# Optimization experiments

Measured on AMD Instinct MI355X. Metric: run time of the kernel, lower is better.

The kernel has to match this reference:

```python
import jax, jax.numpy as jnp
import numpy as np

D_MODEL = 768
KERNELS = [7, 5, 3]
FILTERS = [40, 30, 20]
FC_IN = sum(FILTERS)  # 90


def setup_inputs() -> dict:
    key = jax.random.key(0)
    ks = jax.random.split(key, 16)
    B, S, D = 8, 2048, D_MODEL
    inp = {
        'x1': jax.random.normal(ks[0], (B, S, D), jnp.float32),
        'x2': jax.random.normal(ks[1], (B, S, D), jnp.float32),
    }
    # conv weights: OIH layout [out_ch, in_ch, k]
    for i, (k, f) in enumerate(zip(KERNELS, FILTERS)):
        scale = 1.0 / np.sqrt(D * k)
        inp[f'w{k}'] = jax.random.uniform(ks[2 + 2 * i], (f, D, k), jnp.float32, -scale, scale)
        inp[f'b{k}'] = jax.random.uniform(ks[3 + 2 * i], (f,), jnp.float32, -scale, scale)
    inp['U'] = jax.random.normal(ks[8], (D, D), jnp.float32) * (1.0 / np.sqrt(D))
    inp['bias_v'] = jax.random.normal(ks[9], (D,), jnp.float32) * 0.02
    inp['fc_w'] = jax.random.normal(ks[10], (D, FC_IN), jnp.float32) * (1.0 / np.sqrt(FC_IN))
    inp['fc_b'] = jnp.zeros((D,), jnp.float32)
    inp['fcx_w'] = jax.random.normal(ks[11], (D, 2 * D), jnp.float32) * (1.0 / np.sqrt(2 * D))
    inp['fcx_b'] = jnp.zeros((D,), jnp.float32)
    return inp


def _conv1d_same(x_ncs, w_oik, b_o, k):
    # x: [B, C, S], w: [O, C, k] -> [B, O, S], 'same' padding = k//2
    y = jax.lax.conv_general_dilated(
        x_ncs, w_oik, window_strides=(1,), padding=[(k // 2, k // 2)],
        dimension_numbers=('NCH', 'OIH', 'NCH'))
    return y + b_o[None, :, None]


def reference(x1, x2, w7, b7, w5, b5, w3, b3, U, bias_v, fc_w, fc_b, fcx_w, fcx_b):
    # CNN branch over x2 (dropout layers are identity in eval mode)
    xc = jnp.transpose(x2, (0, 2, 1))  # [B, D, S]
    feats = jnp.concatenate([
        jnp.transpose(_conv1d_same(xc, w7, b7, 7), (0, 2, 1)),
        jnp.transpose(_conv1d_same(xc, w5, b5, 5), (0, 2, 1)),
        jnp.transpose(_conv1d_same(xc, w3, b3, 3), (0, 2, 1)),
    ], axis=-1)                                    # [B, S, 90]
    x = jnp.tanh(jax.nn.relu(feats) @ fc_w.T + fc_b)  # [B, S, D]
    # biaffine attention: x1 @ U @ x2^T + x2 @ bias (broadcast over rows)
    attn = jnp.einsum('bsd,de,bte->bst', x1, U, x2) + (x2 @ bias_v)[:, None, :]
    attn = jax.nn.softmax(attn, axis=-1)           # [B, S, S]
    out = jnp.tanh(attn @ x2)                      # [B, S, D]
    x = x + out
    return jnp.concatenate([x1, x], axis=-1) @ fcx_w.T + fcx_b  # [B, S, D]
```

## Files before the change

### kernel.cpp

```cpp
#include <hip/hip_runtime.h>
#include <cmath>

#define D_MODEL 768
#define SEQ 2048
#define BATCH 8
#define FC_PAD 96
#define FC_PAD2 128
#define KCOMB (7 * D_MODEL)
#define KCHUNK 2688
#define NT_SC (D_MODEL / 64)

typedef unsigned short ushort_t;
typedef _Float16 half_t;
typedef __attribute__((ext_vector_type(8))) _Float16 f16x8;
typedef __attribute__((ext_vector_type(8))) unsigned short u16x8;
typedef __attribute__((ext_vector_type(4))) unsigned short u16x4;
typedef __attribute__((ext_vector_type(4))) float f32x4;

struct Ptr8 { const ushort_t* p[8]; };

__device__ __forceinline__ ushort_t f2h(float x) {
    half_t h = (half_t)x;
    return __builtin_bit_cast(ushort_t, h);
}
__device__ __forceinline__ float h2f(ushort_t u) {
    return (float)__builtin_bit_cast(half_t, u);
}
__device__ __forceinline__ float fast_tanh(float x) {
    float a = fabsf(x);
    float t = __expf(-2.f * a);
    float r = (1.f - t) / (1.f + t);
    return copysignf(r, x);
}
__device__ __forceinline__ void gload16(const ushort_t* g, ushort_t* lbase) {
    __builtin_amdgcn_global_load_lds((const __attribute__((address_space(1))) void*)g,
                                     (__attribute__((address_space(3))) void*)lbase,
                                     16, 0, 0);
}

__global__ void convert_f16_kernel(const float* __restrict__ src, ushort_t* __restrict__ dst, size_t n4) {
    size_t i = (size_t)blockIdx.x * 256 + threadIdx.x;
    if (i >= n4) return;
    f32x4 x = *(const f32x4*)(src + i * 4);
    u16x4 h;
    #pragma unroll
    for (int j = 0; j < 4; ++j) h[j] = f2h(x[j]);
    *(u16x4*)(dst + i * 4) = h;
}

__global__ void convert_fc_kernel(const float* __restrict__ src, ushort_t* __restrict__ dst) {
    int i = blockIdx.x * 256 + threadIdx.x;
    if (i >= D_MODEL * FC_PAD2) return;
    int o = i / FC_PAD2, j = i - o * FC_PAD2;
    dst[i] = (j < 90) ? f2h(src[o * 90 + j]) : 0;
}

__global__ void convert_ut_kernel(const float* __restrict__ U, ushort_t* __restrict__ dst) {
    int i = blockIdx.x * 256 + threadIdx.x;
    if (i >= D_MODEL * D_MODEL) return;
    int n = i / D_MODEL, k = i - n * D_MODEL;
    dst[i] = f2h(U[(size_t)k * D_MODEL + n]);
}

__global__ void build_wcomb_kernel(const float* __restrict__ w7, const float* __restrict__ b7,
                                   const float* __restrict__ w5, const float* __restrict__ b5,
                                   const float* __restrict__ w3, const float* __restrict__ b3,
                                   ushort_t* __restrict__ Wt, float* __restrict__ bcat) {
    int idx = blockIdx.x * 256 + threadIdx.x;
    const int total = FC_PAD2 * KCOMB;
    if (idx < total) {
        int o = idx / KCOMB, k = idx - o * KCOMB;
        int t = k / D_MODEL, d = k - t * D_MODEL;
        float v = 0.f;
        if (o < 40) {
            v = w7[(size_t)o * (D_MODEL * 7) + d * 7 + t];
        } else if (o < 70) {
            int t5 = t - 1;
            if (t5 >= 0 && t5 < 5) v = w5[(size_t)(o - 40) * (D_MODEL * 5) + d * 5 + t5];
        } else if (o < 90) {
            int t3 = t - 2;
            if (t3 >= 0 && t3 < 3) v = w3[(size_t)(o - 70) * (D_MODEL * 3) + d * 3 + t3];
        }
        Wt[idx] = f2h(v);
    }
    if (idx < FC_PAD2) {
        float bv = 0.f;
        if (idx < 40) bv = b7[idx];
        else if (idx < 70) bv = b5[idx - 40];
        else if (idx < 90) bv = b3[idx - 70];
        bcat[idx] = bv;
    }
}

__global__ void conv_reduce_kernel(const float* __restrict__ P, const float* __restrict__ bcat,
                                   ushort_t* __restrict__ feats) {
    const size_t MT = (size_t)BATCH * SEQ;
    size_t i = (size_t)blockIdx.x * 256 + threadIdx.x;
    if (i >= MT * FC_PAD2) return;
    int col = (int)(i & (FC_PAD2 - 1));
    size_t row = i >> 7;
    float v = 0.f;
    if (col < FC_PAD) {
        size_t idx = row * FC_PAD + col;
        const size_t st = MT * FC_PAD;
        v = P[idx] + P[idx + st] + bcat[col];
        v = fmaxf(v, 0.f);
    }
    feats[i] = f2h(v);
}

__global__ void transpose_f16_kernel(const ushort_t* __restrict__ in, ushort_t* __restrict__ out) {
    __shared__ ushort_t tile[32][40];
    int b = blockIdx.z;
    int s0 = blockIdx.x * 32, d0 = blockIdx.y * 32;
    int tx = threadIdx.x & 31, ty = threadIdx.x >> 5;
    const ushort_t* inb = in + (size_t)b * SEQ * D_MODEL;
    ushort_t* outb = out + (size_t)b * D_MODEL * SEQ;
    #pragma unroll
    for (int i = 0; i < 4; ++i)
        tile[ty + i * 8][tx] = inb[(size_t)(s0 + ty + i * 8) * D_MODEL + d0 + tx];
    __syncthreads();
    #pragma unroll
    for (int i = 0; i < 4; ++i)
        outb[(size_t)(d0 + ty + i * 8) * SEQ + s0 + tx] = tile[tx][ty + i * 8];
}

__global__ __launch_bounds__(512, 2)
void scores_kernel(const ushort_t* __restrict__ Abase, const ushort_t* __restrict__ Bbase,
                   Ptr8 ap, float* __restrict__ smw, float* __restrict__ slw) {
    __shared__ __align__(16) ushort_t As_[2][2][256][32];
    __shared__ __align__(16) ushort_t Bs_[2][2][256][32];
    __shared__ float pmW[4][256];
    __shared__ float msS[256];
    __shared__ float plW[4][256];

    const int lin = blockIdx.x;
    const int z = lin & 7;
    const int t6 = lin >> 3;
    const int bx = t6 & 7, by = t6 >> 3;
    const ushort_t* A = Abase + (size_t)z * SEQ * D_MODEL;
    const ushort_t* B = Bbase + (size_t)z * SEQ * D_MODEL;
    const int m0 = bx * 256, n0 = by * 256;

    const int tid = threadIdx.x;
    const int lane = tid & 63;
    const int wave = tid >> 6;
    const int wm2 = wave >> 2;
    const int wn4 = wave & 3;
    const int r16 = lane & 15, kq = lane >> 4;
    const int srow = tid >> 2;
    const int sslot = tid & 3;

    auto swz3 = [](int row) { return (row & 3) ^ ((row >> 2) & 1); };

    auto STAGE = [&](int buf, int kh, int kbase) {
        #pragma unroll
        for (int i = 0; i < 2; ++i) {
            int row = i * 128 + srow;
            int gk = kbase + kh * 32 + ((sslot ^ swz3(row)) << 3);
            gload16(A + (size_t)(m0 + row) * D_MODEL + gk, &As_[buf][kh][i * 128 + wave * 16][0]);
        }
        #pragma unroll
        for (int i = 0; i < 2; ++i) {
            int row = i * 128 + srow;
            int gk = kbase + kh * 32 + ((sslot ^ swz3(row)) << 3);
            gload16(B + (size_t)(n0 + row) * D_MODEL + gk, &Bs_[buf][kh][i * 128 + wave * 16][0]);
        }
    };

    f32x4 acc[8][4];
    #pragma unroll
    for (int i = 0; i < 8; ++i)
        #pragma unroll
        for (int j = 0; j < 4; ++j) acc[i][j] = (f32x4){0.f, 0.f, 0.f, 0.f};

    STAGE(0, 0, 0);
    STAGE(0, 1, 0);
    asm volatile("s_waitcnt vmcnt(0)" ::: "memory");
    __builtin_amdgcn_sched_barrier(0);
    __builtin_amdgcn_s_barrier();
    __builtin_amdgcn_sched_barrier(0);

    for (int t = 0; t < NT_SC; ++t) {
        const int buf = t & 1;
        const int kbn = (t + 1) * 64;
        #pragma unroll
        for (int kk = 0; kk < 2; ++kk) {
            f16x8 af[8], bf[4];
            #pragma unroll
            for (int mi = 0; mi < 8; ++mi) {
                int row = wm2 * 128 + mi * 16 + r16;
                af[mi] = *(const f16x8*)&As_[buf][kk][row][(kq ^ swz3(row)) << 3];
            }
            #pragma unroll
            for (int ni = 0; ni < 4; ++ni) {
                int row = wn4 * 64 + ni * 16 + r16;
                bf[ni] = *(const f16x8*)&Bs_[buf][kk][row][(kq ^ swz3(row)) << 3];
            }
            if (t + 1 < NT_SC) STAGE(buf ^ 1, kk, kbn);
            asm volatile("s_waitcnt vmcnt(4)" ::: "memory");
            asm volatile("s_waitcnt lgkmcnt(0)" ::: "memory");
            __builtin_amdgcn_sched_barrier(0);
            __builtin_amdgcn_s_setprio(1);
            #pragma unroll
            for (int mi = 0; mi < 8; ++mi)
                #pragma unroll
                for (int ni = 0; ni < 4; ++ni)
                    acc[mi][ni] = __builtin_amdgcn_mfma_f32_16x16x32_f16(af[mi], bf[ni], acc[mi][ni], 0, 0, 0);
            __builtin_amdgcn_s_setprio(0);
            __builtin_amdgcn_sched_barrier(0);
            __builtin_amdgcn_s_barrier();
            __builtin_amdgcn_sched_barrier(0);
        }
    }

    float red[8][4];
    #pragma unroll
    for (int mi = 0; mi < 8; ++mi)
        #pragma unroll
        for (int r = 0; r < 4; ++r) {
            float mx = fmaxf(fmaxf(acc[mi][0][r], acc[mi][1][r]), fmaxf(acc[mi][2][r], acc[mi][3][r]));
            mx = fmaxf(mx, __shfl_xor(mx, 1));
            mx = fmaxf(mx, __shfl_xor(mx, 2));
            mx = fmaxf(mx, __shfl_xor(mx, 4));
            mx = fmaxf(mx, __shfl_xor(mx, 8));
            red[mi][r] = mx;
        }
    if (r16 == 0) {
        #pragma unroll
        for (int mi = 0; mi < 8; ++mi)
            #pragma unroll
            for (int r = 0; r < 4; ++r)
                pmW[wn4][wm2 * 128 + mi * 16 + kq * 4 + r] = red[mi][r];
    }
    __syncthreads();
    if (tid < 256)
        msS[tid] = fmaxf(fmaxf(pmW[0][tid], pmW[1][tid]), fmaxf(pmW[2][tid], pmW[3][tid]));
    __syncthreads();
    #pragma unroll
    for (int mi = 0; mi < 8; ++mi)
        #pragma unroll
        for (int r = 0; r < 4; ++r) {
            float m = msS[wm2 * 128 + mi * 16 + kq * 4 + r];
            float s = 0.f;
            #pragma unroll
            for (int ni = 0; ni < 4; ++ni) {
                float e = __expf(acc[mi][ni][r] - m);
                acc[mi][ni][r] = e;
                s += e;
            }
            s += __shfl_xor(s, 1);
            s += __shfl_xor(s, 2);
            s += __shfl_xor(s, 4);
            s += __shfl_xor(s, 8);
            red[mi][r] = s;
        }
    if (r16 == 0) {
        #pragma unroll
        for (int mi = 0; mi < 8; ++mi)
            #pragma unroll
            for (int r = 0; r < 4; ++r)
                plW[wn4][wm2 * 128 + mi * 16 + kq * 4 + r] = red[mi][r];
    }
    __syncthreads();
    if (tid < 256) {
        float l = plW[0][tid] + plW[1][tid] + plW[2][tid] + plW[3][tid];
        size_t si = ((size_t)z * 8 + by) * SEQ + (m0 + tid);
        smw[si] = msS[tid];
        slw[si] = l;
    }
    ushort_t* Co = (ushort_t*)ap.p[z];
    #pragma unroll
    for (int mi = 0; mi < 8; ++mi)
        #pragma unroll
        for (int ni = 0; ni < 4; ++ni)
            #pragma unroll
            for (int r = 0; r < 4; ++r) {
                int gm = m0 + wm2 * 128 + mi * 16 + kq * 4 + r;
                int gn = n0 + wn4 * 64 + ni * 16 + r16;
                Co[(size_t)gm * SEQ + gn] = f2h(acc[mi][ni][r]);
            }
}

template<int TM, int TN, int AMODE, int ACT, int HASBIAS, int HASADD,
         int OUTMODE, int KSPLIT, int APTR, int MAP, int ZM, int GX, int GY,
         int ASCALE>
__global__ __launch_bounds__(256, 4)
void mfma_gemm(const ushort_t* __restrict__ A, const ushort_t* __restrict__ A2,
               const ushort_t* __restrict__ B, const float* __restrict__ bias,
               const ushort_t* __restrict__ addsrc,
               float* __restrict__ Cf, ushort_t* __restrict__ Ch,
               Ptr8 ap, const float* __restrict__ smw, const float* __restrict__ slw,
               int M, int N, int K, int lda, int ldb, int ldc,
               size_t sA, size_t sB, size_t sBias, size_t sC) {
    constexpr int WM = TM / 2, WN = TN / 2, FM = WM / 16, FN = WN / 16;
    __shared__ __align__(16) ushort_t As_[TM * 64];
    __shared__ __align__(16) ushort_t Bs_[TN * 64];
    __shared__ ushort_t alS[ASCALE ? 8 : 1][ASCALE ? 128 : 1];

    int bx, by, z;
    if (MAP == 1) {
        int lin = blockIdx.x;
        z = lin % ZM;
        int t = lin / ZM;
        bx = t % GX;
        by = t / GX;
    } else if (MAP == 2) {
        int lin = blockIdx.x;
        int xcd = lin & 7;
        int t = lin >> 3;
        by = t % GY;
        bx = xcd * (GX / 8) + t / GY;
        z = 0;
    } else if (MAP == 3) {
        int lin = blockIdx.x;
        z = lin % ZM;
        int t = lin / ZM;
        by = t % GY;
        bx = t / GY;
    } else {
        bx = blockIdx.x; by = blockIdx.y; z = blockIdx.z;
    }

    const int kb = KSPLIT ? z * K : 0;
    const ushort_t* Ab = APTR ? ap.p[z] : (A + (KSPLIT ? 0 : (size_t)z * sA));
    const ushort_t* Bb = B + (KSPLIT ? 0 : (size_t)z * sB);
    if (HASBIAS) bias += (size_t)z * sBias;
    if (HASADD) addsrc += (size_t)z * sC;
    if (OUTMODE == 0) Cf += (size_t)z * sC;
    else Ch += (size_t)z * sC;

    const int m0 = bx * TM;
    const int n0 = by * TN;
    const int tid = threadIdx.x;
    const int lane = tid & 63;
    const int wave = tid >> 6;
    const int wm = (wave >> 1) * WM, wn = (wave & 1) * WN;
    const int r16 = lane & 15, kq = lane >> 4;
    const int srow = tid >> 3;
    const int slot = tid & 7;

    if (ASCALE) {
        if (tid < 128) {
            int row = tid;
            int gm = m0 + row;
            float mt[8], al[8];
            float mg = -3.0e38f;
            #pragma unroll
            for (int t = 0; t < 8; ++t) {
                mt[t] = smw[((size_t)z * 8 + t) * SEQ + gm];
                mg = fmaxf(mg, mt[t]);
            }
            float lg = 0.f;
            #pragma unroll
            for (int t = 0; t < 8; ++t) {
                float e = __expf(mt[t] - mg);
                lg += slw[((size_t)z * 8 + t) * SEQ + gm] * e;
                al[t] = e;
            }
            float inv = 1.f / lg;
            #pragma unroll
            for (int t = 0; t < 8; ++t) alS[t][row] = f2h(al[t] * inv);
        }
        __syncthreads();
    }

    f32x4 acc[FM][FN];
    #pragma unroll
    for (int i = 0; i < FM; ++i)
        #pragma unroll
        for (int j = 0; j < FN; ++j) acc[i][j] = (f32x4){0.f, 0.f, 0.f, 0.f};

    const u16x8 zv = {0, 0, 0, 0, 0, 0, 0, 0};

    for (int k0 = 0; k0 < K; k0 += 64) {
        #pragma unroll
        for (int i = 0; i < TM / 32; ++i) {
            int row = i * 32 + srow;
            int gm = m0 + row;
            int xs = slot ^ (row & 7);
            if (AMODE == 1) {
                int gkk = kb + k0 + xs * 8;
                int t = gkk / D_MODEL, d = gkk - t * D_MODEL;
                int s = (gm & (SEQ - 1)) + t - 3;
                int bb = gm >> 11;
                u16x8 v = (s >= 0 && s < SEQ) ? *(const u16x8*)(Ab + ((size_t)(bb * SEQ + s)) * lda + d) : zv;
                *(u16x8*)&As_[(size_t)row * 64 + slot * 8] = v;
            } else {
                const ushort_t* src;
                if (AMODE == 2) {
                    int gk = k0 + xs * 8;
                    src = (gk < D_MODEL) ? Ab + (size_t)gm * D_MODEL + gk
                                         : A2 + (size_t)gm * D_MODEL + (gk - D_MODEL);
                } else {
                    int gk = kb + k0 + xs * 8;
                    src = Ab + (size_t)gm * lda + gk;
                }
                gload16(src, &As_[(size_t)(i * 32 + wave * 8) * 64]);
            }
        }
        #pragma unroll
        for (int i = 0; i < TN / 32; ++i) {
            int row = i * 32 + srow;
            int gn = n0 + row;
            int xs = slot ^ (row & 7);
            int gk = kb + k0 + xs * 8;
            gload16(Bb + (size_t)gn * ldb + gk, &Bs_[(size_t)(i * 32 + wave * 8) * 64]);
        }
        __syncthreads();

        f16x8 ah[FM][2], bh[FN][2];
        #pragma unroll
        for (int mi = 0; mi < FM; ++mi) {
            int row = wm + mi * 16 + r16;
            #pragma unroll
            for (int kk = 0; kk < 2; ++kk)
                ah[mi][kk] = *(const f16x8*)&As_[(size_t)row * 64 + (((kk * 4 + kq) ^ (row & 7)) * 8)];
        }
        if (ASCALE) {
            const int kt = k0 >> 8;
            #pragma unroll
            for (int mi = 0; mi < FM; ++mi) {
                half_t s = __builtin_bit_cast(half_t, alS[kt][wm + mi * 16 + r16]);
                ah[mi][0] = ah[mi][0] * s;
                ah[mi][1] = ah[mi][1] * s;
            }
        }
        #pragma unroll
        for (int ni = 0; ni < FN; ++ni) {
            int row = wn + ni * 16 + r16;
            #pragma unroll
            for (int kk = 0; kk < 2; ++kk)
                bh[ni][kk] = *(const f16x8*)&Bs_[(size_t)row * 64 + (((kk * 4 + kq) ^ (row & 7)) * 8)];
        }
        #pragma unroll
        for (int kk = 0; kk < 2; ++kk)
            #pragma unroll
            for (int mi = 0; mi < FM; ++mi)
                #pragma unroll
                for (int ni = 0; ni < FN; ++ni)
                    acc[mi][ni] = __builtin_amdgcn_mfma_f32_16x16x32_f16(ah[mi][kk], bh[ni][kk], acc[mi][ni], 0, 0, 0);
        __syncthreads();
    }

    #pragma unroll
    for (int mi = 0; mi < FM; ++mi)
        #pragma unroll
        for (int ni = 0; ni < FN; ++ni)
            #pragma unroll
            for (int r = 0; r < 4; ++r) {
                int gm = m0 + wm + mi * 16 + kq * 4 + r;
                int gn = n0 + wn + ni * 16 + r16;
                if (gn >= N) continue;
                float v = acc[mi][ni][r];
                if (HASBIAS) v += bias[gn];
                if (ACT == 1) v = fmaxf(v, 0.f);
                else if (ACT == 2) v = fast_tanh(v);
                if (HASADD) v += h2f(addsrc[(size_t)gm * ldc + gn]);
                size_t idx = (size_t)gm * ldc + gn;
                if (OUTMODE == 0) Cf[idx] = v;
                else Ch[idx] = f2h(v);
            }
}

extern "C" void kernel_launch(void* const* d_in, const int* in_sizes, int n_in,
                              void* d_out, int out_size, void* d_ws, size_t ws_size,
                              hipStream_t stream) {
    const float* x1     = (const float*)d_in[0];
    const float* x2     = (const float*)d_in[1];
    const float* w7     = (const float*)d_in[2];
    const float* b7     = (const float*)d_in[3];
    const float* w5     = (const float*)d_in[4];
    const float* b5     = (const float*)d_in[5];
    const float* w3     = (const float*)d_in[6];
    const float* b3     = (const float*)d_in[7];
    const float* U      = (const float*)d_in[8];
    const float* bias_v = (const float*)d_in[9];
    const float* fc_w   = (const float*)d_in[10];
    const float* fc_b   = (const float*)d_in[11];
    const float* fcx_w  = (const float*)d_in[12];
    const float* fcx_b  = (const float*)d_in[13];
    float* out = (float*)d_out;

    const size_t MT = (size_t)BATCH * SEQ;
    const size_t NE = MT * D_MODEL;
    const size_t NEb = (size_t)SEQ * D_MODEL;
    const size_t SEGSZ = (size_t)SEQ * SEQ;

    char* p = (char*)d_ws;
    auto alloc = [&](size_t bytes) -> char* {
        char* r = p;
        p += (bytes + 255) & ~(size_t)255;
        return r;
    };
    ushort_t* x1_h   = (ushort_t*)alloc(NE * 2);
    ushort_t* x2_h   = (ushort_t*)alloc(NE * 2);
    ushort_t* x2t    = (ushort_t*)alloc(NE * 2);
    ushort_t* y1     = (ushort_t*)alloc(NE * 2);
    ushort_t* xcnn   = (ushort_t*)alloc(NE * 2);
    float*    convp  = (float*)   alloc(MT * FC_PAD * 4 * 4);
    ushort_t* feats  = (ushort_t*)alloc(MT * FC_PAD2 * 2);
    ushort_t* Wt     = (ushort_t*)alloc((size_t)FC_PAD2 * KCOMB * 2);
    ushort_t* fc_wt  = (ushort_t*)alloc((size_t)D_MODEL * FC_PAD2 * 2);
    ushort_t* fcx_wt = (ushort_t*)alloc((size_t)D_MODEL * 2 * D_MODEL * 2);
    ushort_t* Ut     = (ushort_t*)alloc((size_t)D_MODEL * D_MODEL * 2);
    float*    bcat   = (float*)alloc(FC_PAD2 * 4);
    float*    smS    = (float*)alloc((size_t)BATCH * 8 * SEQ * 4);
    float*    slS    = (float*)alloc((size_t)BATCH * 8 * SEQ * 4);

    ushort_t* dob = (ushort_t*)d_out;
    Ptr8 ap;
    ap.p[0] = (ushort_t*)convp;
    ap.p[1] = (ushort_t*)convp + SEGSZ;
    ap.p[2] = (ushort_t*)convp + 2 * SEGSZ;
    ap.p[3] = dob;
    ap.p[4] = dob + SEGSZ;
    ap.p[5] = dob + 2 * SEGSZ;
    ap.p[6] = dob + 3 * SEGSZ;
    ap.p[7] = dob + 4 * SEGSZ;
    Ptr8 apz = {};

    const int T = 256;
    auto blk = [](size_t n) { return dim3((unsigned)((n + 255) / 256)); };

    build_wcomb_kernel<<<blk((size_t)FC_PAD2 * KCOMB), T, 0, stream>>>(w7, b7, w5, b5, w3, b3, Wt, bcat);
    convert_fc_kernel<<<blk((size_t)D_MODEL * FC_PAD2), T, 0, stream>>>(fc_w, fc_wt);
    convert_f16_kernel<<<blk((size_t)D_MODEL * 2 * D_MODEL / 4), T, 0, stream>>>(fcx_w, fcx_wt, (size_t)D_MODEL * 2 * D_MODEL / 4);
    convert_ut_kernel<<<blk((size_t)D_MODEL * D_MODEL), T, 0, stream>>>(U, Ut);
    convert_f16_kernel<<<blk(NE / 4), T, 0, stream>>>(x1, x1_h, NE / 4);
    convert_f16_kernel<<<blk(NE / 4), T, 0, stream>>>(x2, x2_h, NE / 4);
    transpose_f16_kernel<<<dim3(SEQ / 32, D_MODEL / 32, BATCH), T, 0, stream>>>(x2_h, x2t);

    mfma_gemm<64, 128, 1, 0, 0, 0, 0, 1, 0, 0, 1, 1, 1, 0><<<dim3(MT / 64, 1, 2), T, 0, stream>>>(
        x2_h, nullptr, Wt, nullptr, nullptr,
        convp, nullptr, apz, nullptr, nullptr,
        (int)MT, FC_PAD, KCHUNK, D_MODEL, KCOMB, FC_PAD,
        0, 0, 0, MT * FC_PAD);
    conv_reduce_kernel<<<blk(MT * FC_PAD2), T, 0, stream>>>(convp, bcat, feats);

    mfma_gemm<128, 128, 0, 2, 1, 0, 1, 0, 0, 2, 1, 128, 6, 0><<<dim3(768, 1, 1), T, 0, stream>>>(
        feats, nullptr, fc_wt, fc_b, nullptr,
        nullptr, xcnn, apz, nullptr, nullptr,
        (int)MT, D_MODEL, FC_PAD2, FC_PAD2, FC_PAD2, D_MODEL, 0, 0, 0, 0);

    mfma_gemm<128, 128, 0, 0, 1, 0, 1, 0, 0, 2, 1, 128, 6, 0><<<dim3(768, 1, 1), T, 0, stream>>>(
        x1_h, nullptr, Ut, bias_v, nullptr,
        nullptr, y1, apz, nullptr, nullptr,
        (int)MT, D_MODEL, D_MODEL, D_MODEL, D_MODEL, D_MODEL, 0, 0, 0, 0);

    scores_kernel<<<dim3(512, 1, 1), dim3(512), 0, stream>>>(y1, x2_h, ap, smS, slS);

    mfma_gemm<128, 128, 0, 2, 0, 1, 1, 0, 1, 3, 8, 16, 6, 1><<<dim3(768, 1, 1), T, 0, stream>>>(
        nullptr, nullptr, x2t, nullptr,
        xcnn,
        nullptr, xcnn, ap, smS, slS,
        SEQ, D_MODEL, SEQ, SEQ, SEQ, D_MODEL,
        0, NEb, 0, NEb);

    mfma_gemm<128, 128, 2, 0, 1, 0, 0, 0, 0, 2, 1, 128, 6, 0><<<dim3(768, 1, 1), T, 0, stream>>>(
        x1_h, xcnn, fcx_wt, fcx_b, nullptr,
        out, nullptr, apz, nullptr, nullptr,
        (int)MT, D_MODEL, 2 * D_MODEL, D_MODEL, 2 * D_MODEL, D_MODEL, 0, 0, 0, 0);
}
```

Baseline: 346.7 us.

## Retile scores kernel to 256x128 with triple-buffered 64-wide K pipeline

The scores GEMM tile shrinks from 256x256 to 256x128, which doubles the grid to 1024 blocks. The K loop now stages full 64-wide slices into a three-deep LDS ring with XOR swizzle, so loads run two tiles ahead. Partial softmax statistics now come in 16 column chunks instead of 8, and the consumer GEMM's per-chunk scale logic is updated to match. In exchange, each wave holds fewer accumulators and does less operand reuse, there is more partial-stat traffic, and launch bounds drop to one block per CU.

```diff
diff --git a/kernel.cpp b/kernel.cpp
--- a/kernel.cpp
+++ b/kernel.cpp
@@ -8,7 +8,7 @@
 #define FC_PAD2 128
 #define KCOMB (7 * D_MODEL)
 #define KCHUNK 2688
-#define NT_SC (D_MODEL / 64)
+#define NKT 12
 
 typedef unsigned short ushort_t;
 typedef _Float16 half_t;
@@ -125,14 +125,14 @@
         outb[(size_t)(d0 + ty + i * 8) * SEQ + s0 + tx] = tile[tx][ty + i * 8];
 }
 
-__global__ __launch_bounds__(512, 2)
+__global__ __launch_bounds__(512, 1)
 void scores_kernel(const ushort_t* __restrict__ Abase, const ushort_t* __restrict__ Bbase,
                    Ptr8 ap, float* __restrict__ smw, float* __restrict__ slw) {
-    __shared__ __align__(16) ushort_t As_[2][2][256][32];
-    __shared__ __align__(16) ushort_t Bs_[2][2][256][32];
-    __shared__ float pmW[4][256];
+    __shared__ __align__(16) ushort_t As_[3][256][64];
+    __shared__ __align__(16) ushort_t Bs_[3][128][64];
+    __shared__ float pmW[2][256];
     __shared__ float msS[256];
-    __shared__ float plW[4][256];
+    __shared__ float plW[2][256];
 
     const int lin = blockIdx.x;
     const int z = lin & 7;
@@ -140,83 +140,89 @@
     const int bx = t6 & 7, by = t6 >> 3;
     const ushort_t* A = Abase + (size_t)z * SEQ * D_MODEL;
     const ushort_t* B = Bbase + (size_t)z * SEQ * D_MODEL;
-    const int m0 = bx * 256, n0 = by * 256;
+    const int m0 = bx * 256, n0 = by * 128;
 
     const int tid = threadIdx.x;
     const int lane = tid & 63;
     const int wave = tid >> 6;
-    const int wm2 = wave >> 2;
-    const int wn4 = wave & 3;
+    const int wm4 = wave >> 1;
+    const int wn2 = wave & 1;
     const int r16 = lane & 15, kq = lane >> 4;
-    const int srow = tid >> 2;
-    const int sslot = tid & 3;
-
-    auto swz3 = [](int row) { return (row & 3) ^ ((row >> 2) & 1); };
-
-    auto STAGE = [&](int buf, int kh, int kbase) {
+    const int srow = tid >> 3;
+    const int slot = tid & 7;
+
+    auto STAGE = [&](int buf, int kt) {
+        #pragma unroll
+        for (int i = 0; i < 4; ++i) {
+            int row = i * 64 + srow;
+            int xs = slot ^ (row & 7);
+            gload16(A + (size_t)(m0 + row) * D_MODEL + kt * 64 + xs * 8,
+                    &As_[buf][i * 64 + wave * 8][0]);
+        }
         #pragma unroll
         for (int i = 0; i < 2; ++i) {
-            int row = i * 128 + srow;
-            int gk = kbase + kh * 32 + ((sslot ^ swz3(row)) << 3);
-            gload16(A + (size_t)(m0 + row) * D_MODEL + gk, &As_[buf][kh][i * 128 + wave * 16][0]);
-        }
-        #pragma unroll
-        for (int i = 0; i < 2; ++i) {
-            int row = i * 128 + srow;
-            int gk = kbase + kh * 32 + ((sslot ^ swz3(row)) << 3);
-            gload16(B + (size_t)(n0 + row) * D_MODEL + gk, &Bs_[buf][kh][i * 128 + wave * 16][0]);
+            int row = i * 64 + srow;
+            int xs = slot ^ (row & 7);
+            gload16(B + (size_t)(n0 + row) * D_MODEL + kt * 64 + xs * 8,
+                    &Bs_[buf][i * 64 + wave * 8][0]);
         }
     };
 
-    f32x4 acc[8][4];
-    #pragma unroll
-    for (int i = 0; i < 8; ++i)
+    f32x4 acc[4][4];
+    #pragma unroll
+    for (int i = 0; i < 4; ++i)
         #pragma unroll
         for (int j = 0; j < 4; ++j) acc[i][j] = (f32x4){0.f, 0.f, 0.f, 0.f};
 
-    STAGE(0, 0, 0);
-    STAGE(0, 1, 0);
-    asm volatile("s_waitcnt vmcnt(0)" ::: "memory");
+    STAGE(0, 0);
+    STAGE(1, 1);
+    asm volatile("s_waitcnt vmcnt(6)" ::: "memory");
     __builtin_amdgcn_sched_barrier(0);
     __builtin_amdgcn_s_barrier();
     __builtin_amdgcn_sched_barrier(0);
 
-    for (int t = 0; t < NT_SC; ++t) {
-        const int buf = t & 1;
-        const int kbn = (t + 1) * 64;
-        #pragma unroll
-        for (int kk = 0; kk < 2; ++kk) {
-            f16x8 af[8], bf[4];
-            #pragma unroll
-            for (int mi = 0; mi < 8; ++mi) {
-                int row = wm2 * 128 + mi * 16 + r16;
-                af[mi] = *(const f16x8*)&As_[buf][kk][row][(kq ^ swz3(row)) << 3];
-            }
-            #pragma unroll
-            for (int ni = 0; ni < 4; ++ni) {
-                int row = wn4 * 64 + ni * 16 + r16;
-                bf[ni] = *(const f16x8*)&Bs_[buf][kk][row][(kq ^ swz3(row)) << 3];
-            }
-            if (t + 1 < NT_SC) STAGE(buf ^ 1, kk, kbn);
-            asm volatile("s_waitcnt vmcnt(4)" ::: "memory");
-            asm volatile("s_waitcnt lgkmcnt(0)" ::: "memory");
-            __builtin_amdgcn_sched_barrier(0);
-            __builtin_amdgcn_s_setprio(1);
-            #pragma unroll
-            for (int mi = 0; mi < 8; ++mi)
+    for (int t = 0; t < NKT; ++t) {
+        const int buf = t % 3;
+        f16x8 af[4][2], bf[4][2];
+        #pragma unroll
+        for (int mi = 0; mi < 4; ++mi) {
+            int row = wm4 * 64 + mi * 16 + r16;
+            #pragma unroll
+            for (int kk = 0; kk < 2; ++kk)
+                af[mi][kk] = *(const f16x8*)&As_[buf][row][((kk * 4 + kq) ^ (row & 7)) * 8];
+        }
+        #pragma unroll
+        for (int ni = 0; ni < 4; ++ni) {
+            int row = wn2 * 64 + ni * 16 + r16;
+            #pragma unroll
+            for (int kk = 0; kk < 2; ++kk)
+                bf[ni][kk] = *(const f16x8*)&Bs_[buf][row][((kk * 4 + kq) ^ (row & 7)) * 8];
+        }
+        if (t + 2 < NKT) {
+            STAGE((t + 2) % 3, t + 2);
+            asm volatile("s_waitcnt vmcnt(6)" ::: "memory");
+        } else {
+            asm volatile("s_waitcnt vmcnt(0)" ::: "memory");
+        }
+        asm volatile("s_waitcnt lgkmcnt(0)" ::: "memory");
+        __builtin_amdgcn_sched_barrier(0);
+        __builtin_amdgcn_s_setprio(1);
+        #pragma unroll
+        for (int kk = 0; kk < 2; ++kk)
+            #pragma unroll
+            for (int mi = 0; mi < 4; ++mi)
                 #pragma unroll
                 for (int ni = 0; ni < 4; ++ni)
-                    acc[mi][ni] = __builtin_amdgcn_mfma_f32_16x16x32_f16(af[mi], bf[ni], acc[mi][ni], 0, 0, 0);
-            __builtin_amdgcn_s_setprio(0);
-            __builtin_amdgcn_sched_barrier(0);
-            __builtin_amdgcn_s_barrier();
-            __builtin_amdgcn_sched_barrier(0);
-        }
-    }
-
-    float red[8][4];
-    #pragma unroll
-    for (int mi = 0; mi < 8; ++mi)
+                    acc[mi][ni] = __builtin_amdgcn_mfma_f32_16x16x32_f16(af[mi][kk], bf[ni][kk], acc[mi][ni], 0, 0, 0);
+        __builtin_amdgcn_s_setprio(0);
+        __builtin_amdgcn_sched_barrier(0);
+        __builtin_amdgcn_s_barrier();
+        __builtin_amdgcn_sched_barrier(0);
+    }
+
+    float red[4][4];
+    #pragma unroll
+    for (int mi = 0; mi < 4; ++mi)
         #pragma unroll
         for (int r = 0; r < 4; ++r) {
             float mx = fmaxf(fmaxf(acc[mi][0][r], acc[mi][1][r]), fmaxf(acc[mi][2][r], acc[mi][3][r]));
@@ -228,20 +234,19 @@
         }
     if (r16 == 0) {
         #pragma unroll
-        for (int mi = 0; mi < 8; ++mi)
+        for (int mi = 0; mi < 4; ++mi)
             #pragma unroll
             for (int r = 0; r < 4; ++r)
-                pmW[wn4][wm2 * 128 + mi * 16 + kq * 4 + r] = red[mi][r];
+                pmW[wn2][wm4 * 64 + mi * 16 + kq * 4 + r] = red[mi][r];
     }
     __syncthreads();
-    if (tid < 256)
-        msS[tid] = fmaxf(fmaxf(pmW[0][tid], pmW[1][tid]), fmaxf(pmW[2][tid], pmW[3][tid]));
+    if (tid < 256) msS[tid] = fmaxf(pmW[0][tid], pmW[1][tid]);
     __syncthreads();
     #pragma unroll
-    for (int mi = 0; mi < 8; ++mi)
+    for (int mi = 0; mi < 4; ++mi)
         #pragma unroll
         for (int r = 0; r < 4; ++r) {
-            float m = msS[wm2 * 128 + mi * 16 + kq * 4 + r];
+            float m = msS[wm4 * 64 + mi * 16 + kq * 4 + r];
             float s = 0.f;
             #pragma unroll
             for (int ni = 0; ni < 4; ++ni) {
@@ -257,27 +262,27 @@
         }
     if (r16 == 0) {
         #pragma unroll
-        for (int mi = 0; mi < 8; ++mi)
+        for (int mi = 0; mi < 4; ++mi)
             #pragma unroll
             for (int r = 0; r < 4; ++r)
-                plW[wn4][wm2 * 128 + mi * 16 + kq * 4 + r] = red[mi][r];
+                plW[wn2][wm4 * 64 + mi * 16 + kq * 4 + r] = red[mi][r];
     }
     __syncthreads();
     if (tid < 256) {
-        float l = plW[0][tid] + plW[1][tid] + plW[2][tid] + plW[3][tid];
-        size_t si = ((size_t)z * 8 + by) * SEQ + (m0 + tid);
+        float l = plW[0][tid] + plW[1][tid];
+        size_t si = ((size_t)z * 16 + by) * SEQ + (m0 + tid);
         smw[si] = msS[tid];
         slw[si] = l;
     }
     ushort_t* Co = (ushort_t*)ap.p[z];
     #pragma unroll
-    for (int mi = 0; mi < 8; ++mi)
+    for (int mi = 0; mi < 4; ++mi)
         #pragma unroll
         for (int ni = 0; ni < 4; ++ni)
             #pragma unroll
             for (int r = 0; r < 4; ++r) {
-                int gm = m0 + wm2 * 128 + mi * 16 + kq * 4 + r;
-                int gn = n0 + wn4 * 64 + ni * 16 + r16;
+                int gm = m0 + wm4 * 64 + mi * 16 + kq * 4 + r;
+                int gn = n0 + wn2 * 64 + ni * 16 + r16;
                 Co[(size_t)gm * SEQ + gn] = f2h(acc[mi][ni][r]);
             }
 }
@@ -296,7 +301,7 @@
     constexpr int WM = TM / 2, WN = TN / 2, FM = WM / 16, FN = WN / 16;
     __shared__ __align__(16) ushort_t As_[TM * 64];
     __shared__ __align__(16) ushort_t Bs_[TN * 64];
-    __shared__ ushort_t alS[ASCALE ? 8 : 1][ASCALE ? 128 : 1];
+    __shared__ ushort_t alS[ASCALE ? 16 : 1][ASCALE ? 128 : 1];
 
     int bx, by, z;
     if (MAP == 1) {
@@ -344,23 +349,23 @@
         if (tid < 128) {
             int row = tid;
             int gm = m0 + row;
-            float mt[8], al[8];
+            float mt[16], al[16];
             float mg = -3.0e38f;
             #pragma unroll
-            for (int t = 0; t < 8; ++t) {
-                mt[t] = smw[((size_t)z * 8 + t) * SEQ + gm];
+            for (int t = 0; t < 16; ++t) {
+                mt[t] = smw[((size_t)z * 16 + t) * SEQ + gm];
                 mg = fmaxf(mg, mt[t]);
             }
             float lg = 0.f;
             #pragma unroll
-            for (int t = 0; t < 8; ++t) {
+            for (int t = 0; t < 16; ++t) {
                 float e = __expf(mt[t] - mg);
-                lg += slw[((size_t)z * 8 + t) * SEQ + gm] * e;
+                lg += slw[((size_t)z * 16 + t) * SEQ + gm] * e;
                 al[t] = e;
             }
             float inv = 1.f / lg;
             #pragma unroll
-            for (int t = 0; t < 8; ++t) alS[t][row] = f2h(al[t] * inv);
+            for (int t = 0; t < 16; ++t) alS[t][row] = f2h(al[t] * inv);
         }
         __syncthreads();
     }
@@ -418,7 +423,7 @@
                 ah[mi][kk] = *(const f16x8*)&As_[(size_t)row * 64 + (((kk * 4 + kq) ^ (row & 7)) * 8)];
         }
         if (ASCALE) {
-            const int kt = k0 >> 8;
+            const int kt = k0 >> 7;
             #pragma unroll
             for (int mi = 0; mi < FM; ++mi) {
                 half_t s = __builtin_bit_cast(half_t, alS[kt][wm + mi * 16 + r16]);
@@ -505,8 +510,8 @@
     ushort_t* fcx_wt = (ushort_t*)alloc((size_t)D_MODEL * 2 * D_MODEL * 2);
     ushort_t* Ut     = (ushort_t*)alloc((size_t)D_MODEL * D_MODEL * 2);
     float*    bcat   = (float*)alloc(FC_PAD2 * 4);
-    float*    smS    = (float*)alloc((size_t)BATCH * 8 * SEQ * 4);
-    float*    slS    = (float*)alloc((size_t)BATCH * 8 * SEQ * 4);
+    float*    smS    = (float*)alloc((size_t)BATCH * 16 * SEQ * 4);
+    float*    slS    = (float*)alloc((size_t)BATCH * 16 * SEQ * 4);
 
     ushort_t* dob = (ushort_t*)d_out;
     Ptr8 ap;
@@ -548,7 +553,7 @@
         nullptr, y1, apz, nullptr, nullptr,
         (int)MT, D_MODEL, D_MODEL, D_MODEL, D_MODEL, D_MODEL, 0, 0, 0, 0);
 
-    scores_kernel<<<dim3(512, 1, 1), dim3(512), 0, stream>>>(y1, x2_h, ap, smS, slS);
+    scores_kernel<<<dim3(1024, 1, 1), dim3(512), 0, stream>>>(y1, x2_h, ap, smS, slS);
 
     mfma_gemm<128, 128, 0, 2, 0, 1, 1, 0, 1, 3, 8, 16, 6, 1><<<dim3(768, 1, 1), T, 0, stream>>>(
         nullptr, nullptr, x2t, nullptr,
```

Result: no change. 353.1 us (+1.9%).
